# Kernel tuning notes

Measured on AMD Instinct MI355X. Metric: run time of the kernel, lower is better.

The kernel has to match this reference:

```python
import jax, jax.numpy as jnp
import numpy as np

B = 256
NUM_PRIMARY = 32      # cfg.num_primary_caps
PRIM_ATOMS = 8
NUM_CLASSES = 10
DIGIT_ATOMS = 16
NUM_ROUTING = 3       # cfg.num_routing (DigitCap)
IN_DIM = 6 * 6 * NUM_PRIMARY  # 1152
NUM_PIXELS = 28 * 28 * 1


def squash(s, axis):
    # v = ||s||^2/(1+||s||^2) * s/||s||
    n2 = jnp.sum(jnp.square(s), axis=axis, keepdims=True)
    return s * (n2 / (1.0 + n2)) / jnp.sqrt(n2 + 1e-9)


def conv2d(x, w, stride):
    return jax.lax.conv_general_dilated(
        x, w, (stride, stride), 'VALID',
        dimension_numbers=('NCHW', 'OIHW', 'NCHW'))


def setup_inputs() -> dict:
    key = jax.random.key(0)
    ks = jax.random.split(key, 10)
    x = jax.random.uniform(ks[0], (B, 1, 28, 28), jnp.float32)
    labels = jax.random.randint(ks[1], (B,), 0, NUM_CLASSES)
    y = jax.nn.one_hot(labels, NUM_CLASSES, dtype=jnp.float32)
    conv1_w = 0.05 * jax.random.normal(ks[2], (256, 1, 9, 9), jnp.float32)
    conv1_b = jnp.full((256,), 0.1, jnp.float32)
    # primary capsule conv: 256 -> 32 caps * 8 atoms, k=9, s=2 (bias applied after routing)
    prim_w = 0.05 * jax.random.normal(ks[3], (NUM_PRIMARY * PRIM_ATOMS, 256, 9, 9), jnp.float32)
    prim_b = jnp.full((NUM_PRIMARY, PRIM_ATOMS), 0.1, jnp.float32)
    # digit capsule transform: [in_dim, in_atoms, out_dim, out_atoms]
    digit_w = 0.05 * jax.random.normal(ks[4], (IN_DIM, PRIM_ATOMS, NUM_CLASSES, DIGIT_ATOMS), jnp.float32)
    digit_b = jnp.full((NUM_CLASSES, DIGIT_ATOMS), 0.1, jnp.float32)
    w1 = 0.05 * jax.random.normal(ks[5], (NUM_CLASSES * DIGIT_ATOMS, 512), jnp.float32)
    b1 = jnp.zeros((512,), jnp.float32)
    w2 = 0.05 * jax.random.normal(ks[6], (512, 1024), jnp.float32)
    b2 = jnp.zeros((1024,), jnp.float32)
    w3 = 0.05 * jax.random.normal(ks[7], (1024, NUM_PIXELS), jnp.float32)
    b3 = jnp.zeros((NUM_PIXELS,), jnp.float32)
    return dict(x=x, y=y, conv1_w=conv1_w, conv1_b=conv1_b, prim_w=prim_w,
                prim_b=prim_b, digit_w=digit_w, digit_b=digit_b,
                w1=w1, b1=b1, w2=w2, b2=b2, w3=w3, b3=b3)


def reference(x, y, conv1_w, conv1_b, prim_w, prim_b, digit_w, digit_b,
              w1, b1, w2, b2, w3, b3):
    # conv stem
    h = jax.nn.relu(conv2d(x, conv1_w, 1) + conv1_b[None, :, None, None])  # [B,256,20,20]

    # PrimaryCap: conv votes [B, in_dim=1, out=32, atoms=8, 6, 6]; num_routing=1
    votes_p = conv2d(h, prim_w, 2).reshape(B, NUM_PRIMARY, PRIM_ATOMS, 6, 6)
    # one routing iter, input_dim=1: softmax(zeros) over output_dim -> uniform 1/32
    preact_p = votes_p / NUM_PRIMARY + prim_b[None, :, :, None, None]
    caps1 = squash(preact_p, axis=2)  # [B,32,8,6,6]

    # permute(0,1,3,4,2) then flatten -> [B, 1152, 8]
    x3 = jnp.transpose(caps1, (0, 1, 3, 4, 2)).reshape(B, IN_DIM, PRIM_ATOMS)

    # DigitCap votes: [B, in_dim, out_dim, out_atoms]
    votes = jnp.einsum('bia,iaot->biot', x3, digit_w)
    logits = jnp.zeros((B, IN_DIM, NUM_CLASSES), votes.dtype)
    act = None
    for _ in range(NUM_ROUTING):
        route = jax.nn.softmax(logits, axis=2)  # over output capsules
        preact = jnp.einsum('bio,biot->bot', route, votes) + digit_b
        act = squash(preact, axis=-1)  # [B,10,16]
        logits = logits + jnp.einsum('biot,bot->bio', votes, act)
    digit = act

    # Reconstruction: mask by label, 160 -> 512 -> 1024 -> 784
    masked = (digit * y[:, :, None]).reshape(B, NUM_CLASSES * DIGIT_ATOMS)
    r = jax.nn.relu(masked @ w1 + b1)
    r = jax.nn.relu(r @ w2 + b2)
    recon = jax.nn.sigmoid(r @ w3 + b3)
    return digit, recon
```

## Files before the change

kernel.cpp:

```cpp
#include <hip/hip_runtime.h>
#include <hip/hip_bf16.h>

typedef unsigned short u16;
typedef unsigned int u32;

static __device__ __forceinline__ float us2f(u16 u) {
    return __uint_as_float(((u32)u) << 16);
}
static __device__ __forceinline__ u16 f2bu(float f) {
    u32 u = __float_as_uint(f);
    return (u16)((u + 0x7fffu + ((u >> 16) & 1u)) >> 16);
}

typedef __attribute__((ext_vector_type(8))) __bf16 bf16x8;
typedef __attribute__((ext_vector_type(4))) float f32x4;

__global__ void fill_sentinel(float* out, int n, float val) {
    int g = blockIdx.x * 256 + threadIdx.x;
    if (g < n) out[g] = val;
}

__global__ __launch_bounds__(256) void conv_c1wb(const float* __restrict__ w,
                                                 u16* __restrict__ wb)
{
    const int j = blockIdx.x, c = threadIdx.x;
    wb[j * 256 + c] = f2bu(w[c * 81 + j]);
}

__global__ __launch_bounds__(256) void conv1_kernel(const float* __restrict__ x,
    const u16* __restrict__ wb, const float* __restrict__ bias, u16* __restrict__ h)
{
    __shared__ float xs[784];
    __shared__ u16 wl[81 * 256];
    const int b = blockIdx.x >> 2, g = blockIdx.x & 3;
    const int c = threadIdx.x;
    for (int idx = c; idx < 784; idx += 256) xs[idx] = x[b * 784 + idx];
    for (int idx = c; idx < 20736; idx += 256) wl[idx] = wb[idx];
    __syncthreads();
    const float bv = bias[c];
    #pragma unroll 1
    for (int iy = g * 5; iy < g * 5 + 5; ++iy) {
        float acc[20];
        #pragma unroll
        for (int i = 0; i < 20; ++i) acc[i] = bv;
        #pragma unroll 1
        for (int dy = 0; dy < 9; ++dy) {
            float xr[28];
            const float4* xrow = reinterpret_cast<const float4*>(&xs[(iy + dy) * 28]);
            #pragma unroll
            for (int i = 0; i < 7; ++i) {
                float4 v = xrow[i];
                xr[4*i] = v.x; xr[4*i+1] = v.y; xr[4*i+2] = v.z; xr[4*i+3] = v.w;
            }
            #pragma unroll
            for (int dx = 0; dx < 9; ++dx) {
                const float wv = us2f(wl[(dy * 9 + dx) * 256 + c]);
                #pragma unroll
                for (int ix = 0; ix < 20; ++ix) acc[ix] += xr[ix + dx] * wv;
            }
        }
        u16* hp = h + ((b * 20 + iy) * 20) * 256 + c;
        #pragma unroll
        for (int ix = 0; ix < 20; ++ix) hp[ix * 256] = f2bu(fmaxf(acc[ix], 0.f));
    }
}

__global__ __launch_bounds__(256) void transpose_primw(const float* __restrict__ w,
                                                       u16* __restrict__ wt)
{
    __shared__ u16 wl[81 * 258];
    const int n = blockIdx.x, tid = threadIdx.x;
    const float* ws = w + (size_t)n * 20736;
    for (int idx = tid; idx < 20736; idx += 256) {
        const int cc = idx / 81, kk = idx - cc * 81;
        wl[kk * 258 + cc] = f2bu(ws[idx]);
    }
    __syncthreads();
    u16* wo = wt + (size_t)n * 20736;
    for (int q = tid; q < 20736; q += 256)
        wo[q] = wl[(q >> 8) * 258 + (q & 255)];
}

__global__ __launch_bounds__(256) void conv_dwb(const float* __restrict__ dw,
    u16* __restrict__ dwb_t, u16* __restrict__ dwb_a)
{
    const int g = blockIdx.x * 256 + threadIdx.x;
    const float v = dw[g];
    const u16 bv = f2bu(v);
    dwb_t[g] = bv;
    const int i = g / 1280, rem = g % 1280;
    const int a = rem / 160, ot = rem % 160;
    dwb_a[((size_t)i * 160 + ot) * 8 + a] = bv;
}

__global__ __launch_bounds__(256) void prim_gemm_split(const u16* __restrict__ h,
    const u16* __restrict__ wT, float* __restrict__ pm)
{
    __shared__ u16 As[128 * 40];
    __shared__ u16 Bs[128 * 40];
    const int tid = threadIdx.x;
    const int split = blockIdx.y;
    const int mt = blockIdx.x % 72, nt = blockIdx.x / 72;
    const int mBase = mt * 128, nBase = nt * 128;
    const int tq = tid & 3, tr = tid >> 2;
    int m0 = mBase + tr;
    int b0 = m0 / 36, r0 = m0 % 36;
    int aBase0 = ((b0 * 20 + 2 * (r0 / 6)) * 20 + 2 * (r0 % 6)) * 256 + tq * 8;
    int m1 = m0 + 64;
    int b1 = m1 / 36, r1 = m1 % 36;
    int aBase1 = ((b1 * 20 + 2 * (r1 / 6)) * 20 + 2 * (r1 % 6)) * 256 + tq * 8;
    const int bBase0 = (nBase + tr) * 20736 + tq * 8;
    const int bBase1 = (nBase + tr + 64) * 20736 + tq * 8;
    int kglob = split * 1728;
    int ky = kglob / 2304; int krem = kglob - ky * 2304;
    int kx = krem >> 8; int c0 = krem & 255;

    f32x4 acc[4][4];
    #pragma unroll
    for (int i = 0; i < 4; ++i)
        #pragma unroll
        for (int j = 0; j < 4; ++j) acc[i][j] = (f32x4){0.f, 0.f, 0.f, 0.f};

    const int lane = tid & 63;
    const int wvi = tid >> 6; const int wm = wvi >> 1, wn = wvi & 1;
    const int lcol = lane & 15, lquad = lane >> 4;
    const u16* Arow = As + (wm * 64 + lcol) * 40 + lquad * 8;
    const u16* Brow = Bs + (wn * 64 + lcol) * 40 + lquad * 8;

    #pragma unroll 1
    for (int kt = 0; kt < 54; ++kt) {
        const int koffA = (ky * 20 + kx) * 256 + c0;
        uint4 ra0 = *reinterpret_cast<const uint4*>(h + aBase0 + koffA);
        uint4 ra1 = *reinterpret_cast<const uint4*>(h + aBase1 + koffA);
        uint4 rb0 = *reinterpret_cast<const uint4*>(wT + bBase0 + kglob);
        uint4 rb1 = *reinterpret_cast<const uint4*>(wT + bBase1 + kglob);
        __syncthreads();
        *reinterpret_cast<uint4*>(As + tr * 40 + tq * 8)        = ra0;
        *reinterpret_cast<uint4*>(As + (tr + 64) * 40 + tq * 8) = ra1;
        *reinterpret_cast<uint4*>(Bs + tr * 40 + tq * 8)        = rb0;
        *reinterpret_cast<uint4*>(Bs + (tr + 64) * 40 + tq * 8) = rb1;
        __syncthreads();
        bf16x8 af[4], bfr[4];
        #pragma unroll
        for (int i = 0; i < 4; ++i)
            af[i] = *reinterpret_cast<const bf16x8*>(Arow + i * 640);
        #pragma unroll
        for (int j = 0; j < 4; ++j)
            bfr[j] = *reinterpret_cast<const bf16x8*>(Brow + j * 640);
        #pragma unroll
        for (int i = 0; i < 4; ++i)
            #pragma unroll
            for (int j = 0; j < 4; ++j)
                acc[i][j] = __builtin_amdgcn_mfma_f32_16x16x32_bf16(af[i], bfr[j], acc[i][j], 0, 0, 0);
        kglob += 32; c0 += 32;
        if (c0 == 256) { c0 = 0; if (++kx == 9) { kx = 0; ++ky; } }
    }
    #pragma unroll
    for (int i = 0; i < 4; ++i) {
        const int mrow = mBase + wm * 64 + i * 16 + lquad * 4;
        #pragma unroll
        for (int j = 0; j < 4; ++j) {
            const int ncol = nBase + wn * 64 + j * 16 + lcol;
            #pragma unroll
            for (int r = 0; r < 4; ++r)
                unsafeAtomicAdd(&pm[(size_t)(mrow + r) * 256 + ncol], acc[i][j][r]);
        }
    }
}

__global__ __launch_bounds__(256) void squash_kernel(float* __restrict__ pm,
    const float* __restrict__ pb)
{
    const int m = blockIdx.x, t = threadIdx.x;
    float pre = pm[(size_t)m * 256 + t] * (1.f / 32.f) + pb[t];
    float sq = pre * pre;
    sq += __shfl_xor(sq, 1); sq += __shfl_xor(sq, 2); sq += __shfl_xor(sq, 4);
    float scale = (sq / (1.f + sq)) * rsqrtf(sq + 1e-9f);
    pm[(size_t)m * 256 + t] = pre * scale;
}

__global__ __launch_bounds__(256) void routing_act_part(const float* __restrict__ x3m,
    const u16* __restrict__ dwb_a, const float* __restrict__ logits,
    float* __restrict__ preactD, int uniform)
{
    __shared__ float x3s[8192];
    __shared__ float rs[10240];
    const int c = blockIdx.x, bg = blockIdx.y;
    const int tid = threadIdx.x;
    for (int q = tid; q < 8192; q += 256) {
        const int b_l = q >> 10, rest = q & 1023, il = rest >> 3, a = rest & 7;
        const int i = c * 128 + il, cap = i / 36, p = i - cap * 36;
        x3s[q] = x3m[((size_t)(bg * 8 + b_l) * 36 + p) * 256 + cap * 8 + a];
    }
    if (!uniform && tid < 128) {
        const int i = c * 128 + tid;
        for (int b_l = 0; b_l < 8; ++b_l) {
            const float* lg = &logits[((size_t)(bg * 8 + b_l) * 1152 + i) * 10];
            float l[10]; float mx = -1e30f;
            #pragma unroll
            for (int k = 0; k < 10; ++k) { l[k] = lg[k]; mx = fmaxf(mx, l[k]); }
            float s = 0.f;
            #pragma unroll
            for (int k = 0; k < 10; ++k) { l[k] = __expf(l[k] - mx); s += l[k]; }
            const float inv = 1.f / s;
            #pragma unroll
            for (int k = 0; k < 10; ++k) rs[(b_l * 128 + tid) * 10 + k] = l[k] * inv;
        }
    }
    __syncthreads();
    if (tid < 160) {
        const int ot = tid;
        const int o = tid >> 4;
        float preg[8];
        #pragma unroll
        for (int b_l = 0; b_l < 8; ++b_l) preg[b_l] = 0.f;
        #pragma unroll 2
        for (int il = 0; il < 128; ++il) {
            const int i = c * 128 + il;
            const uint4 dq = *reinterpret_cast<const uint4*>(
                &dwb_a[((size_t)i * 160 + ot) * 8]);
            const u32 du[4] = {dq.x, dq.y, dq.z, dq.w};
            float dv[8];
            #pragma unroll
            for (int q = 0; q < 4; ++q) {
                dv[2 * q]     = __uint_as_float(du[q] << 16);
                dv[2 * q + 1] = __uint_as_float(du[q] & 0xffff0000u);
            }
            #pragma unroll
            for (int b_l = 0; b_l < 8; ++b_l) {
                const float* xp = &x3s[(b_l * 128 + il) * 8];
                float v = 0.f;
                #pragma unroll
                for (int a = 0; a < 8; ++a) v += xp[a] * dv[a];
                const float r = uniform ? 0.1f : rs[(b_l * 128 + il) * 10 + o];
                preg[b_l] += r * v;
            }
        }
        #pragma unroll
        for (int b_l = 0; b_l < 8; ++b_l)
            unsafeAtomicAdd(&preactD[(size_t)(bg * 8 + b_l) * 160 + tid], preg[b_l]);
    }
}

__global__ __launch_bounds__(192) void routing_squash(const float* __restrict__ preactD,
    const float* __restrict__ db, float* __restrict__ act, float* __restrict__ dout)
{
    const int b = blockIdx.x, tid = threadIdx.x;
    if (tid < 160) {
        float pre = preactD[(size_t)b * 160 + tid] + db[tid];
        float sq = pre * pre;
        sq += __shfl_xor(sq, 1); sq += __shfl_xor(sq, 2);
        sq += __shfl_xor(sq, 4); sq += __shfl_xor(sq, 8);
        float scale = (sq / (1.f + sq)) * rsqrtf(sq + 1e-9f);
        float a = pre * scale;
        act[(size_t)b * 160 + tid] = a;
        if (dout) dout[(size_t)b * 160 + tid] = a;
    }
}

__global__ __launch_bounds__(256) void routing_upd_part(const float* __restrict__ x3m,
    const u16* __restrict__ dwb_t, const float* __restrict__ act,
    float* __restrict__ logits, int first)
{
    __shared__ float x3s[8192];
    __shared__ float acts[1280];
    const int c = blockIdx.x, bg = blockIdx.y;
    const int tid = threadIdx.x;
    for (int q = tid; q < 8192; q += 256) {
        const int b_l = q >> 10, rest = q & 1023, il = rest >> 3, a = rest & 7;
        const int i = c * 128 + il, cap = i / 36, p = i - cap * 36;
        x3s[q] = x3m[((size_t)(bg * 8 + b_l) * 36 + p) * 256 + cap * 8 + a];
    }
    for (int q = tid; q < 1280; q += 256)
        acts[q] = act[(size_t)(bg * 8 + q / 160) * 160 + (q % 160)];
    __syncthreads();
    const int il = tid >> 1, half = tid & 1;
    const int i = c * 128 + il;
    #pragma unroll 1
    for (int oo = 0; oo < 5; ++oo) {
        const int o = half * 5 + oo;
        float s[8];
        #pragma unroll
        for (int b_l = 0; b_l < 8; ++b_l) s[b_l] = 0.f;
        #pragma unroll
        for (int a = 0; a < 8; ++a) {
            const uint4* dp = reinterpret_cast<const uint4*>(
                &dwb_t[(((size_t)i * 8 + a) * 10 + o) * 16]);
            uint4 d0 = dp[0], d1 = dp[1];
            const u32 du[8] = {d0.x, d0.y, d0.z, d0.w, d1.x, d1.y, d1.z, d1.w};
            #pragma unroll
            for (int b_l = 0; b_l < 8; ++b_l) {
                const float* ap = &acts[b_l * 160 + o * 16];
                float inner = 0.f;
                #pragma unroll
                for (int q = 0; q < 8; ++q) {
                    inner += __uint_as_float(du[q] << 16) * ap[2 * q];
                    inner += __uint_as_float(du[q] & 0xffff0000u) * ap[2 * q + 1];
                }
                s[b_l] += x3s[(b_l * 128 + il) * 8 + a] * inner;
            }
        }
        #pragma unroll
        for (int b_l = 0; b_l < 8; ++b_l) {
            float* lp = &logits[((size_t)(bg * 8 + b_l) * 1152 + i) * 10 + o];
            if (first) *lp = s[b_l]; else *lp += s[b_l];
        }
    }
}

__global__ __launch_bounds__(256) void masked_kernel(const float* __restrict__ act,
    const float* __restrict__ y, float* __restrict__ masked)
{
    const int gid = blockIdx.x * 256 + threadIdx.x;
    const int b = gid / 160, j = gid % 160;
    masked[gid] = act[gid] * y[b * 10 + (j >> 4)];
}

__global__ __launch_bounds__(256) void mlp_layer(const float* __restrict__ in,
    const float* __restrict__ w, const float* __restrict__ bias,
    float* __restrict__ outp, int K, int N, int mode)
{
    __shared__ float ins[2 * 1024];
    const int b0 = blockIdx.x * 2;
    const int n = blockIdx.y * 256 + threadIdx.x;
    for (int idx = threadIdx.x; idx < 2 * K; idx += 256)
        ins[idx] = in[(size_t)b0 * K + idx];
    __syncthreads();
    if (n < N) {
        float a0 = 0.f, a1 = 0.f;
        for (int k = 0; k < K; ++k) {
            const float wvv = w[(size_t)k * N + n];
            a0 += ins[k] * wvv;
            a1 += ins[K + k] * wvv;
        }
        const float bv = bias[n];
        float v[2] = {a0 + bv, a1 + bv};
        #pragma unroll
        for (int j = 0; j < 2; ++j) {
            float xv = v[j];
            xv = (mode == 0) ? fmaxf(xv, 0.f) : 1.f / (1.f + __expf(-xv));
            outp[(size_t)(b0 + j) * N + n] = xv;
        }
    }
}

extern "C" void kernel_launch(void* const* d_in, const int* in_sizes, int n_in,
                              void* d_out, int out_size, void* d_ws, size_t ws_size,
                              hipStream_t stream) {
    const float* x   = (const float*)d_in[0];
    const float* y   = (const float*)d_in[1];
    const float* c1w = (const float*)d_in[2];
    const float* c1b = (const float*)d_in[3];
    const float* pw  = (const float*)d_in[4];
    const float* pb  = (const float*)d_in[5];
    const float* dw  = (const float*)d_in[6];
    const float* db  = (const float*)d_in[7];
    const float* w1  = (const float*)d_in[8];
    const float* b1  = (const float*)d_in[9];
    const float* w2  = (const float*)d_in[10];
    const float* b2  = (const float*)d_in[11];
    const float* w3  = (const float*)d_in[12];
    const float* b3  = (const float*)d_in[13];
    float* out = (float*)d_out;
    char* ws = (char*)d_ws;

    static const int exp_sizes[14] = {200704, 2560, 20736, 256, 5308416, 256,
                                      1474560, 160, 81920, 512, 524288, 1024,
                                      802816, 784};
    int bad = (n_in == 14) ? -1 : -2;
    if (bad == -1)
        for (int i = 0; i < 14; ++i) if (in_sizes[i] != exp_sizes[i]) { bad = i; break; }
    if (bad != -1) {
        fill_sentinel<<<(out_size + 255) / 256, 256, 0, stream>>>(out, out_size,
            7168.f + 16.f * (float)(bad + 1));
        return;
    }
    const size_t NEEDED = 72482816ULL;
    if (ws_size < NEEDED) {
        fill_sentinel<<<(out_size + 255) / 256, 256, 0, stream>>>(out, out_size, 111.0f);
        return;
    }

    u16*   h       = (u16*)(ws);
    u16*   wT2     = (u16*)(ws + 52428800);
    float* x3m     = (float*)(ws + 63045632);
    u16*   c1wb    = (u16*)(ws + 63045632);
    float* logits  = (float*)(ws);
    float* act     = (float*)(ws + 11796480);
    float* masked  = (float*)(ws + 11960320);
    float* r1      = (float*)(ws + 12124160);
    float* r2      = (float*)(ws + 12648448);
    float* preactD = (float*)(ws + 13697024);
    u16*   dwb_t   = (u16*)(ws + 13860864);
    u16*   dwb_a   = (u16*)(ws + 16809984);

    conv_c1wb<<<81, 256, 0, stream>>>(c1w, c1wb);
    conv1_kernel<<<1024, 256, 0, stream>>>(x, c1wb, c1b, h);
    transpose_primw<<<256, 256, 0, stream>>>(pw, wT2);
    hipMemsetAsync(x3m, 0, 9437184, stream);
    prim_gemm_split<<<dim3(144, 12), 256, 0, stream>>>(h, wT2, x3m);
    squash_kernel<<<9216, 256, 0, stream>>>(x3m, pb);
    conv_dwb<<<5760, 256, 0, stream>>>(dw, dwb_t, dwb_a);

    hipMemsetAsync(preactD, 0, 163840, stream);
    routing_act_part<<<dim3(9, 32), 256, 0, stream>>>(x3m, dwb_a, logits, preactD, 1);
    routing_squash<<<256, 192, 0, stream>>>(preactD, db, act, (float*)nullptr);
    routing_upd_part<<<dim3(9, 32), 256, 0, stream>>>(x3m, dwb_t, act, logits, 1);

    hipMemsetAsync(preactD, 0, 163840, stream);
    routing_act_part<<<dim3(9, 32), 256, 0, stream>>>(x3m, dwb_a, logits, preactD, 0);
    routing_squash<<<256, 192, 0, stream>>>(preactD, db, act, (float*)nullptr);
    routing_upd_part<<<dim3(9, 32), 256, 0, stream>>>(x3m, dwb_t, act, logits, 0);

    hipMemsetAsync(preactD, 0, 163840, stream);
    routing_act_part<<<dim3(9, 32), 256, 0, stream>>>(x3m, dwb_a, logits, preactD, 0);
    routing_squash<<<256, 192, 0, stream>>>(preactD, db, act, out);

    masked_kernel<<<160, 256, 0, stream>>>(act, y, masked);
    mlp_layer<<<dim3(128, 2), 256, 0, stream>>>(masked, w1, b1, r1, 160, 512, 0);
    mlp_layer<<<dim3(128, 4), 256, 0, stream>>>(r1, w2, b2, r2, 512, 1024, 0);
    mlp_layer<<<dim3(128, 4), 256, 0, stream>>>(r2, w3, b3, out + 40960, 1024, 784, 1);
}
```

Before: 813.1 us.

## Materialize digit-capsule votes once in bf16 and route over stored votes

Computes the DigitCap votes tensor once per half-batch into a bf16 buffer instead of recomputing x3·W inside every routing act and update pass. The routing act and update kernels then become simple reductions over the stored votes, processed in two half-batches so the buffer fits in the workspace. The mask multiply is folded into the first MLP layer, and the MLP processes four rows per block. The trade is extra memory traffic for a 47 MB votes buffer and bf16 rounding of the votes, in exchange for removing repeated inner products.

```diff
diff --git a/kernel.cpp b/kernel.cpp
--- a/kernel.cpp
+++ b/kernel.cpp
@@ -82,15 +82,10 @@
 }
 
 __global__ __launch_bounds__(256) void conv_dwb(const float* __restrict__ dw,
-    u16* __restrict__ dwb_t, u16* __restrict__ dwb_a)
+                                                u16* __restrict__ dwb_t)
 {
     const int g = blockIdx.x * 256 + threadIdx.x;
-    const float v = dw[g];
-    const u16 bv = f2bu(v);
-    dwb_t[g] = bv;
-    const int i = g / 1280, rem = g % 1280;
-    const int a = rem / 160, ot = rem % 160;
-    dwb_a[((size_t)i * 160 + ot) * 8 + a] = bv;
+    dwb_t[g] = f2bu(dw[g]);
 }
 
 __global__ __launch_bounds__(256) void prim_gemm_split(const u16* __restrict__ h,
@@ -179,73 +174,113 @@
     pm[(size_t)m * 256 + t] = pre * scale;
 }
 
-__global__ __launch_bounds__(256) void routing_act_part(const float* __restrict__ x3m,
-    const u16* __restrict__ dwb_a, const float* __restrict__ logits,
-    float* __restrict__ preactD, int uniform)
-{
-    __shared__ float x3s[8192];
-    __shared__ float rs[10240];
-    const int c = blockIdx.x, bg = blockIdx.y;
+__global__ __launch_bounds__(192) void votes_gemm(const float* __restrict__ x3m,
+    const u16* __restrict__ dwb_t, u16* __restrict__ votes, int hb)
+{
+    __shared__ float dws[8 * 1280];
+    __shared__ float x3s[64 * 64];
+    const int ic = blockIdx.x * 8, bc = blockIdx.y * 64;
     const int tid = threadIdx.x;
-    for (int q = tid; q < 8192; q += 256) {
-        const int b_l = q >> 10, rest = q & 1023, il = rest >> 3, a = rest & 7;
-        const int i = c * 128 + il, cap = i / 36, p = i - cap * 36;
-        x3s[q] = x3m[((size_t)(bg * 8 + b_l) * 36 + p) * 256 + cap * 8 + a];
-    }
-    if (!uniform && tid < 128) {
-        const int i = c * 128 + tid;
-        for (int b_l = 0; b_l < 8; ++b_l) {
-            const float* lg = &logits[((size_t)(bg * 8 + b_l) * 1152 + i) * 10];
-            float l[10]; float mx = -1e30f;
-            #pragma unroll
-            for (int k = 0; k < 10; ++k) { l[k] = lg[k]; mx = fmaxf(mx, l[k]); }
-            float s = 0.f;
-            #pragma unroll
-            for (int k = 0; k < 10; ++k) { l[k] = __expf(l[k] - mx); s += l[k]; }
-            const float inv = 1.f / s;
-            #pragma unroll
-            for (int k = 0; k < 10; ++k) rs[(b_l * 128 + tid) * 10 + k] = l[k] * inv;
-        }
+    for (int q = tid; q < 10240; q += 192)
+        dws[q] = us2f(dwb_t[(size_t)ic * 1280 + q]);
+    for (int q = tid; q < 4096; q += 192) {
+        const int b_l = q >> 6, r = q & 63, i_l = r >> 3, a = r & 7;
+        const int i = ic + i_l, cap = i / 36, p = i - cap * 36;
+        x3s[q] = x3m[((size_t)(hb + bc + b_l) * 36 + p) * 256 + cap * 8 + a];
     }
     __syncthreads();
     if (tid < 160) {
         const int ot = tid;
-        const int o = tid >> 4;
-        float preg[8];
-        #pragma unroll
-        for (int b_l = 0; b_l < 8; ++b_l) preg[b_l] = 0.f;
-        #pragma unroll 2
-        for (int il = 0; il < 128; ++il) {
-            const int i = c * 128 + il;
-            const uint4 dq = *reinterpret_cast<const uint4*>(
-                &dwb_a[((size_t)i * 160 + ot) * 8]);
-            const u32 du[4] = {dq.x, dq.y, dq.z, dq.w};
-            float dv[8];
-            #pragma unroll
-            for (int q = 0; q < 4; ++q) {
-                dv[2 * q]     = __uint_as_float(du[q] << 16);
-                dv[2 * q + 1] = __uint_as_float(du[q] & 0xffff0000u);
-            }
-            #pragma unroll
-            for (int b_l = 0; b_l < 8; ++b_l) {
-                const float* xp = &x3s[(b_l * 128 + il) * 8];
+        float dwr[8][8];
+        #pragma unroll
+        for (int i_l = 0; i_l < 8; ++i_l)
+            #pragma unroll
+            for (int a = 0; a < 8; ++a)
+                dwr[i_l][a] = dws[i_l * 1280 + a * 160 + ot];
+        #pragma unroll 1
+        for (int b_l = 0; b_l < 64; ++b_l) {
+            u16 ob[8];
+            #pragma unroll
+            for (int i_l = 0; i_l < 8; ++i_l) {
+                const float* xp = &x3s[b_l * 64 + i_l * 8];
                 float v = 0.f;
                 #pragma unroll
-                for (int a = 0; a < 8; ++a) v += xp[a] * dv[a];
-                const float r = uniform ? 0.1f : rs[(b_l * 128 + il) * 10 + o];
-                preg[b_l] += r * v;
+                for (int a = 0; a < 8; ++a) v += xp[a] * dwr[i_l][a];
+                ob[i_l] = f2bu(v);
             }
-        }
-        #pragma unroll
-        for (int b_l = 0; b_l < 8; ++b_l)
-            unsafeAtomicAdd(&preactD[(size_t)(bg * 8 + b_l) * 160 + tid], preg[b_l]);
-    }
+            uint4 o4;
+            o4.x = (u32)ob[0] | ((u32)ob[1] << 16);
+            o4.y = (u32)ob[2] | ((u32)ob[3] << 16);
+            o4.z = (u32)ob[4] | ((u32)ob[5] << 16);
+            o4.w = (u32)ob[6] | ((u32)ob[7] << 16);
+            *reinterpret_cast<uint4*>(&votes[((size_t)(bc + b_l) * 160 + ot) * 1152 + ic]) = o4;
+        }
+    }
+}
+
+__global__ __launch_bounds__(256) void routing_act3(const u16* __restrict__ votes,
+    const float* __restrict__ logits, float* __restrict__ preactD, int hb, int uniform)
+{
+    __shared__ float route_s[384 * 10];
+    __shared__ float vs[160 * 65];
+    const int ic = blockIdx.x * 384, b_l = blockIdx.y;
+    const int gb = hb + b_l;
+    const int tid = threadIdx.x;
+    if (!uniform) {
+        for (int q = tid; q < 384; q += 256) {
+            const float* lg = &logits[((size_t)gb * 1152 + ic + q) * 10];
+            float l[10]; float mx = -1e30f;
+            #pragma unroll
+            for (int k = 0; k < 10; ++k) { l[k] = lg[k]; mx = fmaxf(mx, l[k]); }
+            float s = 0.f;
+            #pragma unroll
+            for (int k = 0; k < 10; ++k) { l[k] = __expf(l[k] - mx); s += l[k]; }
+            const float inv = 1.f / s;
+            #pragma unroll
+            for (int k = 0; k < 10; ++k) route_s[q * 10 + k] = l[k] * inv;
+        }
+    }
+    float acc = 0.f;
+    const int o = (tid & 255) >> 4;
+    #pragma unroll 1
+    for (int sc = 0; sc < 6; ++sc) {
+        __syncthreads();
+        for (int q = tid; q < 1280; q += 256) {
+            const int ot = q >> 3, i8 = q & 7;
+            const uint4 d = *reinterpret_cast<const uint4*>(
+                &votes[((size_t)b_l * 160 + ot) * 1152 + ic + sc * 64 + i8 * 8]);
+            const u32 du[4] = {d.x, d.y, d.z, d.w};
+            float* vp = &vs[ot * 65 + i8 * 8];
+            #pragma unroll
+            for (int k = 0; k < 4; ++k) {
+                vp[2 * k]     = __uint_as_float(du[k] << 16);
+                vp[2 * k + 1] = __uint_as_float(du[k] & 0xffff0000u);
+            }
+        }
+        __syncthreads();
+        if (tid < 160) {
+            const float* vrow = &vs[tid * 65];
+            if (uniform) {
+                float s = 0.f;
+                #pragma unroll
+                for (int il = 0; il < 64; ++il) s += vrow[il];
+                acc += 0.1f * s;
+            } else {
+                const float* rp = &route_s[sc * 640 + o];
+                #pragma unroll
+                for (int il = 0; il < 64; ++il)
+                    acc += rp[il * 10] * vrow[il];
+            }
+        }
+    }
+    if (tid < 160)
+        unsafeAtomicAdd(&preactD[(size_t)gb * 160 + tid], acc);
 }
 
 __global__ __launch_bounds__(192) void routing_squash(const float* __restrict__ preactD,
-    const float* __restrict__ db, float* __restrict__ act, float* __restrict__ dout)
-{
-    const int b = blockIdx.x, tid = threadIdx.x;
+    const float* __restrict__ db, float* __restrict__ act, float* __restrict__ dout, int hb)
+{
+    const int b = hb + blockIdx.x, tid = threadIdx.x;
     if (tid < 160) {
         float pre = preactD[(size_t)b * 160 + tid] + db[tid];
         float sq = pre * pre;
@@ -258,85 +293,61 @@
     }
 }
 
-__global__ __launch_bounds__(256) void routing_upd_part(const float* __restrict__ x3m,
-    const u16* __restrict__ dwb_t, const float* __restrict__ act,
-    float* __restrict__ logits, int first)
-{
-    __shared__ float x3s[8192];
-    __shared__ float acts[1280];
-    const int c = blockIdx.x, bg = blockIdx.y;
-    const int tid = threadIdx.x;
-    for (int q = tid; q < 8192; q += 256) {
-        const int b_l = q >> 10, rest = q & 1023, il = rest >> 3, a = rest & 7;
-        const int i = c * 128 + il, cap = i / 36, p = i - cap * 36;
-        x3s[q] = x3m[((size_t)(bg * 8 + b_l) * 36 + p) * 256 + cap * 8 + a];
-    }
-    for (int q = tid; q < 1280; q += 256)
-        acts[q] = act[(size_t)(bg * 8 + q / 160) * 160 + (q % 160)];
+__global__ __launch_bounds__(128) void routing_upd3(const u16* __restrict__ votes,
+    const float* __restrict__ act, float* __restrict__ logits, int hb, int first)
+{
+    __shared__ float act_s[160];
+    const int b_l = blockIdx.y, gb = hb + b_l;
+    const int i = blockIdx.x * 128 + threadIdx.x;
+    for (int q = threadIdx.x; q < 160; q += 128)
+        act_s[q] = act[(size_t)gb * 160 + q];
     __syncthreads();
-    const int il = tid >> 1, half = tid & 1;
-    const int i = c * 128 + il;
-    #pragma unroll 1
-    for (int oo = 0; oo < 5; ++oo) {
-        const int o = half * 5 + oo;
-        float s[8];
-        #pragma unroll
-        for (int b_l = 0; b_l < 8; ++b_l) s[b_l] = 0.f;
-        #pragma unroll
-        for (int a = 0; a < 8; ++a) {
-            const uint4* dp = reinterpret_cast<const uint4*>(
-                &dwb_t[(((size_t)i * 8 + a) * 10 + o) * 16]);
-            uint4 d0 = dp[0], d1 = dp[1];
-            const u32 du[8] = {d0.x, d0.y, d0.z, d0.w, d1.x, d1.y, d1.z, d1.w};
-            #pragma unroll
-            for (int b_l = 0; b_l < 8; ++b_l) {
-                const float* ap = &acts[b_l * 160 + o * 16];
-                float inner = 0.f;
-                #pragma unroll
-                for (int q = 0; q < 8; ++q) {
-                    inner += __uint_as_float(du[q] << 16) * ap[2 * q];
-                    inner += __uint_as_float(du[q] & 0xffff0000u) * ap[2 * q + 1];
-                }
-                s[b_l] += x3s[(b_l * 128 + il) * 8 + a] * inner;
-            }
-        }
-        #pragma unroll
-        for (int b_l = 0; b_l < 8; ++b_l) {
-            float* lp = &logits[((size_t)(bg * 8 + b_l) * 1152 + i) * 10 + o];
-            if (first) *lp = s[b_l]; else *lp += s[b_l];
-        }
-    }
-}
-
-__global__ __launch_bounds__(256) void masked_kernel(const float* __restrict__ act,
-    const float* __restrict__ y, float* __restrict__ masked)
-{
-    const int gid = blockIdx.x * 256 + threadIdx.x;
-    const int b = gid / 160, j = gid % 160;
-    masked[gid] = act[gid] * y[b * 10 + (j >> 4)];
+    float acc[10];
+    #pragma unroll
+    for (int k = 0; k < 10; ++k) acc[k] = 0.f;
+    const u16* vb = &votes[(size_t)b_l * 160 * 1152 + i];
+    #pragma unroll
+    for (int ot = 0; ot < 160; ++ot)
+        acc[ot >> 4] += us2f(vb[(size_t)ot * 1152]) * act_s[ot];
+    float* lp = &logits[((size_t)gb * 1152 + i) * 10];
+    if (first) {
+        #pragma unroll
+        for (int k = 0; k < 10; ++k) lp[k] = acc[k];
+    } else {
+        #pragma unroll
+        for (int k = 0; k < 10; ++k) lp[k] += acc[k];
+    }
 }
 
 __global__ __launch_bounds__(256) void mlp_layer(const float* __restrict__ in,
-    const float* __restrict__ w, const float* __restrict__ bias,
-    float* __restrict__ outp, int K, int N, int mode)
-{
-    __shared__ float ins[2 * 1024];
-    const int b0 = blockIdx.x * 2;
+    const float* __restrict__ maskY, const float* __restrict__ w,
+    const float* __restrict__ bias, float* __restrict__ outp, int K, int N, int mode)
+{
+    __shared__ float ins[4 * 1024];
+    const int b0 = blockIdx.x * 4;
     const int n = blockIdx.y * 256 + threadIdx.x;
-    for (int idx = threadIdx.x; idx < 2 * K; idx += 256)
-        ins[idx] = in[(size_t)b0 * K + idx];
+    for (int idx = threadIdx.x; idx < 4 * K; idx += 256) {
+        float v = in[(size_t)b0 * K + idx];
+        if (maskY) {
+            const int b_l = idx / K, j = idx % K;
+            v *= maskY[(b0 + b_l) * 10 + (j >> 4)];
+        }
+        ins[idx] = v;
+    }
     __syncthreads();
     if (n < N) {
-        float a0 = 0.f, a1 = 0.f;
+        float a0 = 0.f, a1 = 0.f, a2 = 0.f, a3 = 0.f;
         for (int k = 0; k < K; ++k) {
             const float wvv = w[(size_t)k * N + n];
             a0 += ins[k] * wvv;
             a1 += ins[K + k] * wvv;
+            a2 += ins[2 * K + k] * wvv;
+            a3 += ins[3 * K + k] * wvv;
         }
         const float bv = bias[n];
-        float v[2] = {a0 + bv, a1 + bv};
-        #pragma unroll
-        for (int j = 0; j < 2; ++j) {
+        float v[4] = {a0 + bv, a1 + bv, a2 + bv, a3 + bv};
+        #pragma unroll
+        for (int j = 0; j < 4; ++j) {
             float xv = v[j];
             xv = (mode == 0) ? fmaxf(xv, 0.f) : 1.f / (1.f + __expf(-xv));
             outp[(size_t)(b0 + j) * N + n] = xv;
@@ -385,14 +396,13 @@
     u16*   wT2     = (u16*)(ws + 52428800);
     float* x3m     = (float*)(ws + 63045632);
     u16*   c1wb    = (u16*)(ws + 63045632);
-    float* logits  = (float*)(ws);
-    float* act     = (float*)(ws + 11796480);
-    float* masked  = (float*)(ws + 11960320);
-    float* r1      = (float*)(ws + 12124160);
-    float* r2      = (float*)(ws + 12648448);
-    float* preactD = (float*)(ws + 13697024);
-    u16*   dwb_t   = (u16*)(ws + 13860864);
-    u16*   dwb_a   = (u16*)(ws + 16809984);
+    u16*   votes   = (u16*)(ws);
+    float* logits  = (float*)(ws + 47185920);
+    float* act     = (float*)(ws + 58982400);
+    float* preactD = (float*)(ws + 59146240);
+    u16*   dwb_t   = (u16*)(ws + 59637760);
+    float* r1      = (float*)(ws + 62586880);
+    float* r2      = (float*)(ws + 63111168);
 
     conv_c1wb<<<81, 256, 0, stream>>>(c1w, c1wb);
     conv1_kernel<<<1024, 256, 0, stream>>>(x, c1wb, c1b, h);
@@ -400,24 +410,24 @@
     hipMemsetAsync(x3m, 0, 9437184, stream);
     prim_gemm_split<<<dim3(144, 12), 256, 0, stream>>>(h, wT2, x3m);
     squash_kernel<<<9216, 256, 0, stream>>>(x3m, pb);
-    conv_dwb<<<5760, 256, 0, stream>>>(dw, dwb_t, dwb_a);
-
-    hipMemsetAsync(preactD, 0, 163840, stream);
-    routing_act_part<<<dim3(9, 32), 256, 0, stream>>>(x3m, dwb_a, logits, preactD, 1);
-    routing_squash<<<256, 192, 0, stream>>>(preactD, db, act, (float*)nullptr);
-    routing_upd_part<<<dim3(9, 32), 256, 0, stream>>>(x3m, dwb_t, act, logits, 1);
-
-    hipMemsetAsync(preactD, 0, 163840, stream);
-    routing_act_part<<<dim3(9, 32), 256, 0, stream>>>(x3m, dwb_a, logits, preactD, 0);
-    routing_squash<<<256, 192, 0, stream>>>(preactD, db, act, (float*)nullptr);
-    routing_upd_part<<<dim3(9, 32), 256, 0, stream>>>(x3m, dwb_t, act, logits, 0);
-
-    hipMemsetAsync(preactD, 0, 163840, stream);
-    routing_act_part<<<dim3(9, 32), 256, 0, stream>>>(x3m, dwb_a, logits, preactD, 0);
-    routing_squash<<<256, 192, 0, stream>>>(preactD, db, act, out);
-
-    masked_kernel<<<160, 256, 0, stream>>>(act, y, masked);
-    mlp_layer<<<dim3(128, 2), 256, 0, stream>>>(masked, w1, b1, r1, 160, 512, 0);
-    mlp_layer<<<dim3(128, 4), 256, 0, stream>>>(r1, w2, b2, r2, 512, 1024, 0);
-    mlp_layer<<<dim3(128, 4), 256, 0, stream>>>(r2, w3, b3, out + 40960, 1024, 784, 1);
-}
+    conv_dwb<<<5760, 256, 0, stream>>>(dw, dwb_t);
+    hipMemsetAsync(preactD, 0, 491520, stream);
+
+    float* pD0 = preactD, *pD1 = preactD + 40960, *pD2 = preactD + 81920;
+    for (int half = 0; half < 2; ++half) {
+        const int hb = half * 128;
+        votes_gemm<<<dim3(144, 2), 192, 0, stream>>>(x3m, dwb_t, votes, hb);
+        routing_act3<<<dim3(3, 128), 256, 0, stream>>>(votes, logits, pD0, hb, 1);
+        routing_squash<<<128, 192, 0, stream>>>(pD0, db, act, (float*)nullptr, hb);
+        routing_upd3<<<dim3(9, 128), 128, 0, stream>>>(votes, act, logits, hb, 1);
+        routing_act3<<<dim3(3, 128), 256, 0, stream>>>(votes, logits, pD1, hb, 0);
+        routing_squash<<<128, 192, 0, stream>>>(pD1, db, act, (float*)nullptr, hb);
+        routing_upd3<<<dim3(9, 128), 128, 0, stream>>>(votes, act, logits, hb, 0);
+        routing_act3<<<dim3(3, 128), 256, 0, stream>>>(votes, logits, pD2, hb, 0);
+        routing_squash<<<128, 192, 0, stream>>>(pD2, db, act, out, hb);
+    }
+
+    mlp_layer<<<dim3(64, 2), 256, 0, stream>>>(act, y, w1, b1, r1, 160, 512, 0);
+    mlp_layer<<<dim3(64, 4), 256, 0, stream>>>(r1, (float*)nullptr, w2, b2, r2, 512, 1024, 0);
+    mlp_layer<<<dim3(64, 4), 256, 0, stream>>>(r2, (float*)nullptr, w3, b3, out + 40960, 1024, 784, 1);
+}
```

New measurement: 774.4 us. 1.05x faster.
